# Optimization experiments

Hardware: AMD Instinct MI355X
Metric: run time of the kernel (lower is better)

## Reference

```python
import jax, jax.numpy as jnp
import numpy as np

L = 3          # num_legs
D = 32         # leg_dim == out_leg_dim (output_dim = input_dim = D**L)
NUM_NODES = 6  # num_levels * (num_legs - 1) = 3 * 2
B = 256        # batch


def setup_inputs() -> dict:
    key = jax.random.key(0)
    k1, k2 = jax.random.split(key, 2)
    inputs = jax.random.normal(k1, (B, D ** L), dtype=jnp.float32)
    # all 6 entangler nodes share shape (D,D,D,D) since leg_dim == out_leg_dim;
    # scale ~ 1/D to mimic glorot and keep the 6-contraction chain numerically sane
    nodes = jax.random.normal(k2, (NUM_NODES, D, D, D, D), dtype=jnp.float32) / D
    bias = jnp.zeros((D ** L,), dtype=jnp.float32)
    return {"inputs": inputs, "nodes": nodes, "bias": bias}


def reference(inputs, nodes, bias):
    # Faithful port of DenseEntangler.call: reshape the input vector to L legs,
    # then contract NUM_NODES 4-leg tensors; node i eats edge slots (i%L, (i+1)%L)
    # with its axes (0,1) and replaces them with its axes (2,3).
    # jnp.tensordot output axis order (free axes of x in order, then node axes 2,3)
    # matches tn.contract_between's default ordering, so the final flatten is identical.
    Bn = inputs.shape[0]
    x = inputs.reshape((Bn,) + (D,) * L)   # axis 0 = batch, axes 1..L = legs
    pos = list(range(1, L + 1))            # edge slot k -> current axis of x
    for i in range(NUM_NODES):
        s0, s1 = i % L, (i + 1) % L
        p, q = pos[s0], pos[s1]
        x = jnp.tensordot(x, nodes[i], axes=[[p, q], [0, 1]])
        # remaining axes of x keep order (batch stays axis 0); new node axes go last
        new_pos = [0] * L
        for k in range(L):
            if k == s0:
                new_pos[k] = L - 1
            elif k == s1:
                new_pos[k] = L
            else:
                a = pos[k]
                new_pos[k] = a - (p < a) - (q < a)
        pos = new_pos
    out = x.reshape(Bn, -1) + bias  # flatten in current axis order, as in the TF code
    return jax.nn.relu(out)
```

## Files before the change

### kernel.cpp

```cpp
#include <hip/hip_runtime.h>
#include <hip/hip_bf16.h>
#include <stdint.h>

using bf16 = __hip_bfloat16;
typedef __attribute__((ext_vector_type(8))) short short8;
typedef __attribute__((ext_vector_type(4))) float floatx4;

#define DD 32
#define DL3 32768
#define BATCH 256
#define NK 1024

__device__ __forceinline__ void load16(const void* g, void* l) {
  __builtin_amdgcn_global_load_lds((const __attribute__((address_space(1))) void*)g,
                                   (__attribute__((address_space(3))) void*)l,
                                   16, 0, 0);
}

__global__ __launch_bounds__(256) void prep_x(const float* __restrict__ x, bf16* __restrict__ dst) {
  int b = blockIdx.x >> 5, v = blockIdx.x & 31;
  __shared__ float tile[32][33];
  const float* xb = x + (size_t)b * DL3 + v * DD;
  int t = threadIdx.x;
#pragma unroll
  for (int it = 0; it < 4; ++it) {
    int u = (t >> 5) + it * 8, f = t & 31;
    tile[u][f] = xb[u * NK + f];
  }
  __syncthreads();
  bf16* db = dst + (size_t)b * DL3 + v * NK;
#pragma unroll
  for (int it = 0; it < 4; ++it) {
    int f = (t >> 5) + it * 8, u = t & 31;
    db[f * DD + u] = __float2bfloat16(tile[u][f]);
  }
}

__global__ __launch_bounds__(256) void prep_nodes(const float* __restrict__ nodes, bf16* __restrict__ dst) {
  int id = blockIdx.x;
  int nb = id & 31, kb = (id >> 5) & 31, i = id >> 10;
  const float* src = nodes + (size_t)i * 1048576;
  bf16* d = dst + (size_t)i * 1048576;
  __shared__ float tile[32][33];
  int t = threadIdx.x;
#pragma unroll
  for (int it = 0; it < 4; ++it) {
    int u = (t >> 5) + it * 8, j = t & 31;
    tile[u][j] = src[(size_t)(u * 32 + kb) * 1024 + nb * 32 + j];
  }
  __syncthreads();
#pragma unroll
  for (int it = 0; it < 4; ++it) {
    int j = (t >> 5) + it * 8, u = t & 31;
    d[(size_t)(nb * 32 + j) * 1024 + kb * 32 + u] = __float2bfloat16(tile[u][j]);
  }
}

template <bool FINAL>
__global__ __launch_bounds__(256) void entangler_gemm(
    const bf16* __restrict__ A, const bf16* __restrict__ Bn,
    bf16* __restrict__ Cb, float* __restrict__ Cf, const float* __restrict__ bias) {
  __shared__ bf16 sA[4 * 128 * 32];
  __shared__ bf16 sB[4 * 128 * 32];
  const int t = threadIdx.x;
  const int lane = t & 63;
  const int lane16 = lane & 15, quad = lane >> 4;
  const int w = t >> 6;
  const int m0 = (w >> 1) * 64, n0 = (w & 1) * 64;
  const int b0 = blockIdx.x * 4;
  const int N0 = blockIdx.y * 128;

  floatx4 acc[4][4];
#pragma unroll
  for (int i = 0; i < 4; ++i)
#pragma unroll
    for (int j = 0; j < 4; ++j)
      acc[i][j] = (floatx4){0.f, 0.f, 0.f, 0.f};

  const bf16* Ab = A + (size_t)b0 * DL3;
  const bf16* Bb = Bn + (size_t)N0 * NK;

  for (int kv = 0; kv < 8; ++kv) {
    __syncthreads();
#pragma unroll
    for (int r = 0; r < 8; ++r) {
      int e = (r * 256 + t) * 8;
      int vv = e >> 12;
      int bb = (e >> 10) & 3;
      int remA = e & 1023;
      load16(Ab + (size_t)bb * DL3 + (kv * 4 + vv) * NK + remA, sA + e);
      int n = (e >> 5) & 127;
      int u8 = e & 31;
      load16(Bb + (size_t)n * NK + (kv * 4 + vv) * 32 + u8, sB + e);
    }
    __syncthreads();

#pragma unroll
    for (int kk = 0; kk < 4; ++kk) {
      const bf16* pA = sA + kk * 4096;
      const bf16* pB = sB + kk * 4096;
      short8 af[4], bfr[4];
#pragma unroll
      for (int i = 0; i < 4; ++i)
        af[i] = *(const short8*)(pA + (m0 + i * 16 + lane16) * 32 + quad * 8);
#pragma unroll
      for (int j = 0; j < 4; ++j)
        bfr[j] = *(const short8*)(pB + (n0 + j * 16 + lane16) * 32 + quad * 8);
#pragma unroll
      for (int i = 0; i < 4; ++i)
#pragma unroll
        for (int j = 0; j < 4; ++j)
          acc[i][j] = __builtin_amdgcn_mfma_f32_16x16x32_bf16(af[i], bfr[j], acc[i][j], 0, 0, 0);
    }
  }

  const int R0 = blockIdx.x * 128;
#pragma unroll
  for (int i = 0; i < 4; ++i) {
#pragma unroll
    for (int j = 0; j < 4; ++j) {
#pragma unroll
      for (int r = 0; r < 4; ++r) {
        int row = R0 + m0 + i * 16 + quad * 4 + r;
        int col = N0 + n0 + j * 16 + lane16;
        if (FINAL) {
          float v = acc[i][j][r] + bias[(row & 31) * 1024 + col];
          Cf[(size_t)row * 1024 + col] = fmaxf(v, 0.f);
        } else {
          Cb[(size_t)row * 1024 + col] = __float2bfloat16(acc[i][j][r]);
        }
      }
    }
  }
}

extern "C" void kernel_launch(void* const* d_in, const int* in_sizes, int n_in,
                              void* d_out, int out_size, void* d_ws, size_t ws_size,
                              hipStream_t stream) {
  const float* x     = (const float*)d_in[0];
  const float* nodes = (const float*)d_in[1];
  const float* bias  = (const float*)d_in[2];
  float* out = (float*)d_out;

  bf16* buf0  = (bf16*)d_ws;
  bf16* buf1  = buf0 + (size_t)BATCH * DL3;
  bf16* nodeT = buf1 + (size_t)BATCH * DL3;

  prep_x<<<dim3(BATCH * 32), dim3(256), 0, stream>>>(x, buf0);
  prep_nodes<<<dim3(6 * 1024), dim3(256), 0, stream>>>(nodes, nodeT);

  dim3 grid(64, 8), blk(256);
  entangler_gemm<false><<<grid, blk, 0, stream>>>(buf0, nodeT + (size_t)0 * 1048576, buf1, nullptr, nullptr);
  entangler_gemm<false><<<grid, blk, 0, stream>>>(buf1, nodeT + (size_t)1 * 1048576, buf0, nullptr, nullptr);
  entangler_gemm<false><<<grid, blk, 0, stream>>>(buf0, nodeT + (size_t)2 * 1048576, buf1, nullptr, nullptr);
  entangler_gemm<false><<<grid, blk, 0, stream>>>(buf1, nodeT + (size_t)3 * 1048576, buf0, nullptr, nullptr);
  entangler_gemm<false><<<grid, blk, 0, stream>>>(buf0, nodeT + (size_t)4 * 1048576, buf1, nullptr, nullptr);
  entangler_gemm<true ><<<grid, blk, 0, stream>>>(buf1, nodeT + (size_t)5 * 1048576, nullptr, out, bias);
}
```

Before: 233.2 us.

## Double-buffer LDS tiles in entangler GEMM to overlap loads with MFMA

Reorganizes the K loop of the bf16 entangler GEMM from 8 steps of 128-wide K tiles into 16 steps of 64-wide tiles with two LDS buffers. The next tile is fetched via global_load_lds while MFMAs run on the current one. This leaves one barrier per step instead of two and is meant to hide global memory latency behind compute. Total LDS footprint stays the same, but each step now does less MFMA work per barrier, and the overlap relies on the barrier's implicit waitcnt.

```diff
diff --git a/kernel.cpp b/kernel.cpp
--- a/kernel.cpp
+++ b/kernel.cpp
@@ -60,8 +60,8 @@
 __global__ __launch_bounds__(256) void entangler_gemm(
     const bf16* __restrict__ A, const bf16* __restrict__ Bn,
     bf16* __restrict__ Cb, float* __restrict__ Cf, const float* __restrict__ bias) {
-  __shared__ bf16 sA[4 * 128 * 32];
-  __shared__ bf16 sB[4 * 128 * 32];
+  __shared__ bf16 sA[2][8192];
+  __shared__ bf16 sB[2][8192];
   const int t = threadIdx.x;
   const int lane = t & 63;
   const int lane16 = lane & 15, quad = lane >> 4;
@@ -80,25 +80,41 @@
   const bf16* Ab = A + (size_t)b0 * DL3;
   const bf16* Bb = Bn + (size_t)N0 * NK;
 
-  for (int kv = 0; kv < 8; ++kv) {
-    __syncthreads();
+  const bf16* gA[4];
+  const bf16* gB[4];
+  int eoff[4];
 #pragma unroll
-    for (int r = 0; r < 8; ++r) {
-      int e = (r * 256 + t) * 8;
-      int vv = e >> 12;
-      int bb = (e >> 10) & 3;
-      int remA = e & 1023;
-      load16(Ab + (size_t)bb * DL3 + (kv * 4 + vv) * NK + remA, sA + e);
-      int n = (e >> 5) & 127;
-      int u8 = e & 31;
-      load16(Bb + (size_t)n * NK + (kv * 4 + vv) * 32 + u8, sB + e);
-    }
-    __syncthreads();
+  for (int r = 0; r < 4; ++r) {
+    int e = (r * 256 + t) * 8;
+    eoff[r] = e;
+    int vv = e >> 12;
+    int bb = (e >> 10) & 3;
+    int remA = e & 1023;
+    gA[r] = Ab + (size_t)bb * DL3 + vv * NK + remA;
+    int n = (e >> 5) & 127;
+    int u8 = e & 31;
+    gB[r] = Bb + (size_t)n * NK + vv * 32 + u8;
+  }
 
 #pragma unroll
-    for (int kk = 0; kk < 4; ++kk) {
-      const bf16* pA = sA + kk * 4096;
-      const bf16* pB = sB + kk * 4096;
+  for (int r = 0; r < 4; ++r) { load16(gA[r], &sA[0][eoff[r]]); gA[r] += 2 * NK; }
+#pragma unroll
+  for (int r = 0; r < 4; ++r) { load16(gB[r], &sB[0][eoff[r]]); gB[r] += 2 * 32; }
+  __syncthreads();
+
+#pragma unroll
+  for (int kt = 0; kt < 16; ++kt) {
+    const int buf = kt & 1;
+    if (kt < 15) {
+#pragma unroll
+      for (int r = 0; r < 4; ++r) { load16(gA[r], &sA[buf ^ 1][eoff[r]]); gA[r] += 2 * NK; }
+#pragma unroll
+      for (int r = 0; r < 4; ++r) { load16(gB[r], &sB[buf ^ 1][eoff[r]]); gB[r] += 2 * 32; }
+    }
+#pragma unroll
+    for (int kk = 0; kk < 2; ++kk) {
+      const bf16* pA = &sA[buf][kk * 4096];
+      const bf16* pB = &sB[buf][kk * 4096];
       short8 af[4], bfr[4];
 #pragma unroll
       for (int i = 0; i < 4; ++i)
@@ -112,6 +128,7 @@
         for (int j = 0; j < 4; ++j)
           acc[i][j] = __builtin_amdgcn_mfma_f32_16x16x32_bf16(af[i], bfr[j], acc[i][j], 0, 0, 0);
     }
+    if (kt < 15) __syncthreads();
   }
 
   const int R0 = blockIdx.x * 128;
```

Result: no change. 231.3 us (-0.8%).

## Triple-buffer GEMM K-loop with swizzled LDS, split-K warps and larger tiles

Applied to the files above, without the earlier changes.

Rewrites the entangler GEMM to use 256x128 tiles with 512 threads. Global loads go into a three-stage LDS ring with prefetch two steps ahead, so loads overlap the MFMA work. LDS addressing is XOR-swizzled to cut bank conflicts, warps split K in two and reduce their partial sums through LDS, and s_setprio is raised around the MFMA block. The cost is 144 KB of dynamic LDS per block and a grid of only 256 blocks, which may leave CUs underused and adds reduction overhead.

```diff
diff --git a/kernel.cpp b/kernel.cpp
--- a/kernel.cpp
+++ b/kernel.cpp
@@ -10,6 +10,14 @@
 #define DL3 32768
 #define BATCH 256
 #define NK 1024
+
+#define BM 256
+#define BN 128
+#define NKT 16
+#define A_ELEM 16384
+#define B_ELEM 8192
+#define BUF_ELEM 24576
+#define LDS_BYTES 147456
 
 __device__ __forceinline__ void load16(const void* g, void* l) {
   __builtin_amdgcn_global_load_lds((const __attribute__((address_space(1))) void*)g,
@@ -57,77 +65,129 @@
 }
 
 template <bool FINAL>
-__global__ __launch_bounds__(256) void entangler_gemm(
+__global__ __launch_bounds__(512, 2) void entangler_gemm(
     const bf16* __restrict__ A, const bf16* __restrict__ Bn,
     bf16* __restrict__ Cb, float* __restrict__ Cf, const float* __restrict__ bias) {
-  __shared__ bf16 sA[4 * 128 * 32];
-  __shared__ bf16 sB[4 * 128 * 32];
+  extern __shared__ char smem[];
+  bf16* lds = (bf16*)smem;
+
   const int t = threadIdx.x;
   const int lane = t & 63;
   const int lane16 = lane & 15, quad = lane >> 4;
   const int w = t >> 6;
-  const int m0 = (w >> 1) * 64, n0 = (w & 1) * 64;
-  const int b0 = blockIdx.x * 4;
+  const int wm = (w >> 2) & 1, wn = (w >> 1) & 1, wk = w & 1;
+  const int sel = (lane16 >> 1) & 3;
+  const int qs = (quad ^ sel) * 8;
+  const int b0 = blockIdx.x * 8;
   const int N0 = blockIdx.y * 128;
 
-  floatx4 acc[4][4];
-#pragma unroll
-  for (int i = 0; i < 4; ++i)
+  const int aRd = wk * 8192 + (wm * 128 + lane16) * 32 + qs;
+  const int bRd = A_ELEM + wk * 4096 + (wn * 64 + lane16) * 32 + qs;
+
+  int aOff[4], aLds[4], bOff[2], bLds[2];
+#pragma unroll
+  for (int r = 0; r < 4; ++r) {
+    int P = (r * 512 + t) * 16;
+    int L = P ^ (((P >> 7) & 3) << 4);
+    int kk = L >> 14, m = (L >> 6) & 255, u0 = (L & 63) >> 1;
+    aOff[r] = (b0 + (m >> 5)) * DL3 + kk * NK + (m & 31) * 32 + u0;
+    aLds[r] = P >> 1;
+  }
+#pragma unroll
+  for (int r = 0; r < 2; ++r) {
+    int P = (r * 512 + t) * 16;
+    int L = P ^ (((P >> 7) & 3) << 4);
+    int kk = L >> 13, n = (L >> 6) & 127, u0 = (L & 63) >> 1;
+    bOff[r] = (N0 + n) * NK + kk * 32 + u0;
+    bLds[r] = A_ELEM + (P >> 1);
+  }
+
+  floatx4 acc[8][4];
+#pragma unroll
+  for (int i = 0; i < 8; ++i)
 #pragma unroll
     for (int j = 0; j < 4; ++j)
       acc[i][j] = (floatx4){0.f, 0.f, 0.f, 0.f};
 
-  const bf16* Ab = A + (size_t)b0 * DL3;
-  const bf16* Bb = Bn + (size_t)N0 * NK;
-
-  for (int kv = 0; kv < 8; ++kv) {
-    __syncthreads();
-#pragma unroll
-    for (int r = 0; r < 8; ++r) {
-      int e = (r * 256 + t) * 8;
-      int vv = e >> 12;
-      int bb = (e >> 10) & 3;
-      int remA = e & 1023;
-      load16(Ab + (size_t)bb * DL3 + (kv * 4 + vv) * NK + remA, sA + e);
-      int n = (e >> 5) & 127;
-      int u8 = e & 31;
-      load16(Bb + (size_t)n * NK + (kv * 4 + vv) * 32 + u8, sB + e);
-    }
-    __syncthreads();
-
-#pragma unroll
-    for (int kk = 0; kk < 4; ++kk) {
-      const bf16* pA = sA + kk * 4096;
-      const bf16* pB = sB + kk * 4096;
-      short8 af[4], bfr[4];
-#pragma unroll
-      for (int i = 0; i < 4; ++i)
-        af[i] = *(const short8*)(pA + (m0 + i * 16 + lane16) * 32 + quad * 8);
+#pragma unroll
+  for (int s = 0; s < 2; ++s) {
+    bf16* bp = lds + s * BUF_ELEM;
+#pragma unroll
+    for (int r = 0; r < 4; ++r) load16(A + aOff[r] + s * 2048, bp + aLds[r]);
+#pragma unroll
+    for (int r = 0; r < 2; ++r) load16(Bn + bOff[r] + s * 64, bp + bLds[r]);
+  }
+  asm volatile("s_waitcnt vmcnt(6)" ::: "memory");
+  __builtin_amdgcn_s_barrier();
+  asm volatile("" ::: "memory");
+
+#pragma unroll
+  for (int kt = 0; kt < NKT; ++kt) {
+    const bf16* bp = lds + (kt % 3) * BUF_ELEM;
+    short8 af[8], bfr[4];
+#pragma unroll
+    for (int i = 0; i < 8; ++i) af[i] = *(const short8*)(bp + aRd + i * 512);
+#pragma unroll
+    for (int j = 0; j < 4; ++j) bfr[j] = *(const short8*)(bp + bRd + j * 512);
+    if (kt < NKT - 2) {
+      bf16* np = lds + ((kt + 2) % 3) * BUF_ELEM;
+#pragma unroll
+      for (int r = 0; r < 4; ++r) load16(A + aOff[r] + (kt + 2) * 2048, np + aLds[r]);
+#pragma unroll
+      for (int r = 0; r < 2; ++r) load16(Bn + bOff[r] + (kt + 2) * 64, np + bLds[r]);
+    }
+    asm volatile("" ::: "memory");
+    __builtin_amdgcn_s_barrier();
+    asm volatile("" ::: "memory");
+    __builtin_amdgcn_s_setprio(1);
+#pragma unroll
+    for (int i = 0; i < 8; ++i)
 #pragma unroll
       for (int j = 0; j < 4; ++j)
-        bfr[j] = *(const short8*)(pB + (n0 + j * 16 + lane16) * 32 + quad * 8);
-#pragma unroll
-      for (int i = 0; i < 4; ++i)
-#pragma unroll
-        for (int j = 0; j < 4; ++j)
-          acc[i][j] = __builtin_amdgcn_mfma_f32_16x16x32_bf16(af[i], bfr[j], acc[i][j], 0, 0, 0);
-    }
-  }
-
-  const int R0 = blockIdx.x * 128;
-#pragma unroll
-  for (int i = 0; i < 4; ++i) {
-#pragma unroll
-    for (int j = 0; j < 4; ++j) {
-#pragma unroll
-      for (int r = 0; r < 4; ++r) {
-        int row = R0 + m0 + i * 16 + quad * 4 + r;
-        int col = N0 + n0 + j * 16 + lane16;
-        if (FINAL) {
-          float v = acc[i][j][r] + bias[(row & 31) * 1024 + col];
-          Cf[(size_t)row * 1024 + col] = fmaxf(v, 0.f);
-        } else {
-          Cb[(size_t)row * 1024 + col] = __float2bfloat16(acc[i][j][r]);
+        acc[i][j] = __builtin_amdgcn_mfma_f32_16x16x32_bf16(af[i], bfr[j], acc[i][j], 0, 0, 0);
+    __builtin_amdgcn_s_setprio(0);
+    if (kt < NKT - 2) {
+      asm volatile("s_waitcnt vmcnt(6)" ::: "memory");
+    } else if (kt == NKT - 2) {
+      asm volatile("s_waitcnt vmcnt(0)" ::: "memory");
+    }
+    if (kt < NKT - 1) {
+      __builtin_amdgcn_s_barrier();
+      asm volatile("" ::: "memory");
+    }
+  }
+
+  __syncthreads();
+  float* red = (float*)smem;
+  const int pair = (wm << 1) | wn;
+  if (wk == 1) {
+    float* dst = red + pair * 8192;
+#pragma unroll
+    for (int i = 0; i < 8; ++i)
+#pragma unroll
+      for (int j = 0; j < 4; ++j)
+        *(floatx4*)(dst + ((i * 4 + j) * 64 + lane) * 4) = acc[i][j];
+  }
+  __syncthreads();
+  if (wk == 0) {
+    const float* src = red + pair * 8192;
+    const int R0 = blockIdx.x * 256;
+#pragma unroll
+    for (int i = 0; i < 8; ++i) {
+#pragma unroll
+      for (int j = 0; j < 4; ++j) {
+        floatx4 p = *(const floatx4*)(src + ((i * 4 + j) * 64 + lane) * 4);
+        acc[i][j] += p;
+#pragma unroll
+        for (int r = 0; r < 4; ++r) {
+          int row = R0 + wm * 128 + i * 16 + quad * 4 + r;
+          int col = N0 + wn * 64 + j * 16 + lane16;
+          if (FINAL) {
+            float v = acc[i][j][r] + bias[(row & 31) * 1024 + col];
+            Cf[(size_t)row * 1024 + col] = fmaxf(v, 0.f);
+          } else {
+            Cb[(size_t)row * 1024 + col] = __float2bfloat16(acc[i][j][r]);
+          }
         }
       }
     }
@@ -146,14 +206,23 @@
   bf16* buf1  = buf0 + (size_t)BATCH * DL3;
   bf16* nodeT = buf1 + (size_t)BATCH * DL3;
 
+  static bool attr_done = false;
+  if (!attr_done) {
+    hipFuncSetAttribute((const void*)entangler_gemm<false>,
+                        hipFuncAttributeMaxDynamicSharedMemorySize, LDS_BYTES);
+    hipFuncSetAttribute((const void*)entangler_gemm<true>,
+                        hipFuncAttributeMaxDynamicSharedMemorySize, LDS_BYTES);
+    attr_done = true;
+  }
+
   prep_x<<<dim3(BATCH * 32), dim3(256), 0, stream>>>(x, buf0);
   prep_nodes<<<dim3(6 * 1024), dim3(256), 0, stream>>>(nodes, nodeT);
 
-  dim3 grid(64, 8), blk(256);
-  entangler_gemm<false><<<grid, blk, 0, stream>>>(buf0, nodeT + (size_t)0 * 1048576, buf1, nullptr, nullptr);
-  entangler_gemm<false><<<grid, blk, 0, stream>>>(buf1, nodeT + (size_t)1 * 1048576, buf0, nullptr, nullptr);
-  entangler_gemm<false><<<grid, blk, 0, stream>>>(buf0, nodeT + (size_t)2 * 1048576, buf1, nullptr, nullptr);
-  entangler_gemm<false><<<grid, blk, 0, stream>>>(buf1, nodeT + (size_t)3 * 1048576, buf0, nullptr, nullptr);
-  entangler_gemm<false><<<grid, blk, 0, stream>>>(buf0, nodeT + (size_t)4 * 1048576, buf1, nullptr, nullptr);
-  entangler_gemm<true ><<<grid, blk, 0, stream>>>(buf1, nodeT + (size_t)5 * 1048576, nullptr, out, bias);
-}
+  dim3 grid(32, 8), blk(512);
+  entangler_gemm<false><<<grid, blk, LDS_BYTES, stream>>>(buf0, nodeT + (size_t)0 * 1048576, buf1, nullptr, nullptr);
+  entangler_gemm<false><<<grid, blk, LDS_BYTES, stream>>>(buf1, nodeT + (size_t)1 * 1048576, buf0, nullptr, nullptr);
+  entangler_gemm<false><<<grid, blk, LDS_BYTES, stream>>>(buf0, nodeT + (size_t)2 * 1048576, buf1, nullptr, nullptr);
+  entangler_gemm<false><<<grid, blk, LDS_BYTES, stream>>>(buf1, nodeT + (size_t)3 * 1048576, buf0, nullptr, nullptr);
+  entangler_gemm<false><<<grid, blk, LDS_BYTES, stream>>>(buf0, nodeT + (size_t)4 * 1048576, buf1, nullptr, nullptr);
+  entangler_gemm<true ><<<grid, blk, LDS_BYTES, stream>>>(buf1, nodeT + (size_t)5 * 1048576, nullptr, out, bias);
+}
```

New measurement: 231.2 us. Within noise of the previous version (-0.9%).

## Fuse all six entangler contractions into one per-batch kernel with LDS-resident activations

Applied to the files above, without the earlier changes.

Replaces the x-prep kernel and six separate GEMM launches with a single kernel in which each 512-thread block owns one batch sample. The sample's activations stay in swizzled LDS, ping-ponged between two 64 KB buffers across all six stages, while node fragments are read directly from global memory into registers with software prefetch. This removes the global round-trips of intermediate activations and the per-stage launch overhead. In exchange, every block re-reads all node weights from global/L2, LDS use limits occupancy, and only 256 blocks run in total.

```diff
diff --git a/kernel.cpp b/kernel.cpp
--- a/kernel.cpp
+++ b/kernel.cpp
@@ -10,31 +10,7 @@
 #define DL3 32768
 #define BATCH 256
 #define NK 1024
-
-__device__ __forceinline__ void load16(const void* g, void* l) {
-  __builtin_amdgcn_global_load_lds((const __attribute__((address_space(1))) void*)g,
-                                   (__attribute__((address_space(3))) void*)l,
-                                   16, 0, 0);
-}
-
-__global__ __launch_bounds__(256) void prep_x(const float* __restrict__ x, bf16* __restrict__ dst) {
-  int b = blockIdx.x >> 5, v = blockIdx.x & 31;
-  __shared__ float tile[32][33];
-  const float* xb = x + (size_t)b * DL3 + v * DD;
-  int t = threadIdx.x;
-#pragma unroll
-  for (int it = 0; it < 4; ++it) {
-    int u = (t >> 5) + it * 8, f = t & 31;
-    tile[u][f] = xb[u * NK + f];
-  }
-  __syncthreads();
-  bf16* db = dst + (size_t)b * DL3 + v * NK;
-#pragma unroll
-  for (int it = 0; it < 4; ++it) {
-    int f = (t >> 5) + it * 8, u = t & 31;
-    db[f * DD + u] = __float2bfloat16(tile[u][f]);
-  }
-}
+#define LDS_BYTES 131072
 
 __global__ __launch_bounds__(256) void prep_nodes(const float* __restrict__ nodes, bf16* __restrict__ dst) {
   int id = blockIdx.x;
@@ -56,78 +32,120 @@
   }
 }
 
-template <bool FINAL>
-__global__ __launch_bounds__(256) void entangler_gemm(
-    const bf16* __restrict__ A, const bf16* __restrict__ Bn,
-    bf16* __restrict__ Cb, float* __restrict__ Cf, const float* __restrict__ bias) {
-  __shared__ bf16 sA[4 * 128 * 32];
-  __shared__ bf16 sB[4 * 128 * 32];
+__global__ __launch_bounds__(512, 2) void entangler_batch(
+    const float* __restrict__ x, const bf16* __restrict__ nodeT,
+    float* __restrict__ out, const float* __restrict__ bias) {
+  extern __shared__ char smem[];
+  char* st0 = smem;
+  char* st1 = smem + 65536;
+
   const int t = threadIdx.x;
   const int lane = t & 63;
   const int lane16 = lane & 15, quad = lane >> 4;
   const int w = t >> 6;
-  const int m0 = (w >> 1) * 64, n0 = (w & 1) * 64;
-  const int b0 = blockIdx.x * 4;
-  const int N0 = blockIdx.y * 128;
+  const int b = blockIdx.x;
 
-  floatx4 acc[4][4];
+  const float* xb = x + (size_t)b * DL3;
 #pragma unroll
-  for (int i = 0; i < 4; ++i)
+  for (int it = 0; it < 16; ++it) {
+    int flat = it * 512 + t;
+    floatx4 vx = *(const floatx4*)(xb + flat * 4);
+    int e0 = flat * 4;
+    int f = e0 & 31, v = (e0 >> 5) & 31, u = e0 >> 10;
 #pragma unroll
-    for (int j = 0; j < 4; ++j)
-      acc[i][j] = (floatx4){0.f, 0.f, 0.f, 0.f};
-
-  const bf16* Ab = A + (size_t)b0 * DL3;
-  const bf16* Bb = Bn + (size_t)N0 * NK;
-
-  for (int kv = 0; kv < 8; ++kv) {
-    __syncthreads();
-#pragma unroll
-    for (int r = 0; r < 8; ++r) {
-      int e = (r * 256 + t) * 8;
-      int vv = e >> 12;
-      int bb = (e >> 10) & 3;
-      int remA = e & 1023;
-      load16(Ab + (size_t)bb * DL3 + (kv * 4 + vv) * NK + remA, sA + e);
-      int n = (e >> 5) & 127;
-      int u8 = e & 31;
-      load16(Bb + (size_t)n * NK + (kv * 4 + vv) * 32 + u8, sB + e);
-    }
-    __syncthreads();
-
-#pragma unroll
-    for (int kk = 0; kk < 4; ++kk) {
-      const bf16* pA = sA + kk * 4096;
-      const bf16* pB = sB + kk * 4096;
-      short8 af[4], bfr[4];
-#pragma unroll
-      for (int i = 0; i < 4; ++i)
-        af[i] = *(const short8*)(pA + (m0 + i * 16 + lane16) * 32 + quad * 8);
-#pragma unroll
-      for (int j = 0; j < 4; ++j)
-        bfr[j] = *(const short8*)(pB + (n0 + j * 16 + lane16) * 32 + quad * 8);
-#pragma unroll
-      for (int i = 0; i < 4; ++i)
-#pragma unroll
-        for (int j = 0; j < 4; ++j)
-          acc[i][j] = __builtin_amdgcn_mfma_f32_16x16x32_bf16(af[i], bfr[j], acc[i][j], 0, 0, 0);
+    for (int e = 0; e < 4; ++e) {
+      int byte = (v * 1024 + (f + e) * 32 + u) * 2;
+      byte ^= ((byte >> 7) & 3) << 4;
+      *(bf16*)(st0 + byte) = __float2bfloat16(vx[e]);
     }
   }
 
-  const int R0 = blockIdx.x * 128;
+  const bf16* pB[8];
 #pragma unroll
-  for (int i = 0; i < 4; ++i) {
+  for (int j = 0; j < 8; ++j)
+    pB[j] = nodeT + (size_t)(w * 128 + j * 16 + lane16) * 1024 + quad * 8;
+
+  int aAddr[2];
 #pragma unroll
-    for (int j = 0; j < 4; ++j) {
+  for (int i = 0; i < 2; ++i) {
+    int byte = ((i * 16 + lane16) * 32 + quad * 8) * 2;
+    aAddr[i] = byte ^ (((byte >> 7) & 3) << 4);
+  }
+
+  char* sIn = st0;
+  char* sOut = st1;
+  __syncthreads();
+
+#pragma unroll 1
+  for (int s = 0; s < 6; ++s) {
+    floatx4 acc[2][8];
 #pragma unroll
-      for (int r = 0; r < 4; ++r) {
-        int row = R0 + m0 + i * 16 + quad * 4 + r;
-        int col = N0 + n0 + j * 16 + lane16;
-        if (FINAL) {
-          float v = acc[i][j][r] + bias[(row & 31) * 1024 + col];
-          Cf[(size_t)row * 1024 + col] = fmaxf(v, 0.f);
-        } else {
-          Cb[(size_t)row * 1024 + col] = __float2bfloat16(acc[i][j][r]);
+    for (int i = 0; i < 2; ++i)
+#pragma unroll
+      for (int j = 0; j < 8; ++j)
+        acc[i][j] = (floatx4){0.f, 0.f, 0.f, 0.f};
+
+    short8 b0[8], b1[8], af0[2], af1[2];
+#pragma unroll
+    for (int j = 0; j < 8; ++j) b0[j] = *(const short8*)(pB[j] + 0 * 32);
+#pragma unroll 1
+    for (int kc = 0; kc < 32; kc += 2) {
+#pragma unroll
+      for (int j = 0; j < 8; ++j) b1[j] = *(const short8*)(pB[j] + (kc + 1) * 32);
+#pragma unroll
+      for (int i = 0; i < 2; ++i)
+        af0[i] = *(const short8*)(sIn + aAddr[i] + kc * 2048);
+#pragma unroll
+      for (int i = 0; i < 2; ++i)
+#pragma unroll
+        for (int j = 0; j < 8; ++j)
+          acc[i][j] = __builtin_amdgcn_mfma_f32_16x16x32_bf16(af0[i], b0[j], acc[i][j], 0, 0, 0);
+      if (kc + 2 < 32) {
+#pragma unroll
+        for (int j = 0; j < 8; ++j) b0[j] = *(const short8*)(pB[j] + (kc + 2) * 32);
+      }
+#pragma unroll
+      for (int i = 0; i < 2; ++i)
+        af1[i] = *(const short8*)(sIn + aAddr[i] + (kc + 1) * 2048);
+#pragma unroll
+      for (int i = 0; i < 2; ++i)
+#pragma unroll
+        for (int j = 0; j < 8; ++j)
+          acc[i][j] = __builtin_amdgcn_mfma_f32_16x16x32_bf16(af1[i], b1[j], acc[i][j], 0, 0, 0);
+    }
+
+    if (s < 5) {
+#pragma unroll
+      for (int i = 0; i < 2; ++i) {
+#pragma unroll
+        for (int j = 0; j < 8; ++j) {
+#pragma unroll
+          for (int r = 0; r < 4; ++r) {
+            int f = i * 16 + quad * 4 + r;
+            int n = w * 128 + j * 16 + lane16;
+            int byte = (f * 1024 + n) * 2;
+            byte ^= ((byte >> 7) & 3) << 4;
+            *(bf16*)(sOut + byte) = __float2bfloat16(acc[i][j][r]);
+          }
+        }
+      }
+#pragma unroll
+      for (int j = 0; j < 8; ++j) pB[j] += 1048576;
+      __syncthreads();
+      char* tmp = sIn; sIn = sOut; sOut = tmp;
+    } else {
+      float* ob = out + (size_t)b * DL3;
+#pragma unroll
+      for (int i = 0; i < 2; ++i) {
+#pragma unroll
+        for (int j = 0; j < 8; ++j) {
+#pragma unroll
+          for (int r = 0; r < 4; ++r) {
+            int f = i * 16 + quad * 4 + r;
+            int n = w * 128 + j * 16 + lane16;
+            float v = acc[i][j][r] + bias[f * 1024 + n];
+            ob[f * 1024 + n] = fmaxf(v, 0.f);
+          }
         }
       }
     }
@@ -142,18 +160,15 @@
   const float* bias  = (const float*)d_in[2];
   float* out = (float*)d_out;
 
-  bf16* buf0  = (bf16*)d_ws;
-  bf16* buf1  = buf0 + (size_t)BATCH * DL3;
-  bf16* nodeT = buf1 + (size_t)BATCH * DL3;
+  bf16* nodeT = (bf16*)d_ws;
 
-  prep_x<<<dim3(BATCH * 32), dim3(256), 0, stream>>>(x, buf0);
+  static bool attr_done = false;
+  if (!attr_done) {
+    hipFuncSetAttribute((const void*)entangler_batch,
+                        hipFuncAttributeMaxDynamicSharedMemorySize, LDS_BYTES);
+    attr_done = true;
+  }
+
   prep_nodes<<<dim3(6 * 1024), dim3(256), 0, stream>>>(nodes, nodeT);
-
-  dim3 grid(64, 8), blk(256);
-  entangler_gemm<false><<<grid, blk, 0, stream>>>(buf0, nodeT + (size_t)0 * 1048576, buf1, nullptr, nullptr);
-  entangler_gemm<false><<<grid, blk, 0, stream>>>(buf1, nodeT + (size_t)1 * 1048576, buf0, nullptr, nullptr);
-  entangler_gemm<false><<<grid, blk, 0, stream>>>(buf0, nodeT + (size_t)2 * 1048576, buf1, nullptr, nullptr);
-  entangler_gemm<false><<<grid, blk, 0, stream>>>(buf1, nodeT + (size_t)3 * 1048576, buf0, nullptr, nullptr);
-  entangler_gemm<false><<<grid, blk, 0, stream>>>(buf0, nodeT + (size_t)4 * 1048576, buf1, nullptr, nullptr);
-  entangler_gemm<true ><<<grid, blk, 0, stream>>>(buf1, nodeT + (size_t)5 * 1048576, nullptr, out, bias);
+  entangler_batch<<<dim3(BATCH), dim3(512), LDS_BYTES, stream>>>(x, nodeT, out, bias);
 }
```

After: 444.8 us. 90.7% more time.
